# Kernel optimization log

Hardware: AMD Instinct MI355X
Metric: run time of the kernel (lower is better)

The kernel has to match this reference:

```python
import jax, jax.numpy as jnp
import numpy as np

B, NB, H, E, NCT, NL = 16, 4096, 128, 65536, 32, 2
LN_EPS = 1e-5


def _layernorm(x, scale, bias):
    mu = jnp.mean(x, axis=-1, keepdims=True)
    var = jnp.var(x, axis=-1, keepdims=True)
    return (x - mu) / jnp.sqrt(var + LN_EPS) * scale + bias


def setup_inputs() -> dict:
    key = jax.random.key(0)
    ks = jax.random.split(key, 18)
    s = 1.0 / np.sqrt(H)
    inp = {
        'block_tokens': jax.random.normal(ks[0], (B, NB, H), jnp.float32),
        'edge_structure': jnp.full((E,), 0.5, jnp.float32),
        'ct_emb': 0.1 * jax.random.normal(ks[1], (NCT, E), jnp.float32),
        'W_proj': s * jax.random.normal(ks[2], (H, H), jnp.float32),
        'b_proj': jnp.zeros((H,), jnp.float32),
        'W_gate': (1.0 / np.sqrt(2 * H)) * jax.random.normal(ks[3], (2 * H, H), jnp.float32),
        'b_gate': jnp.zeros((H,), jnp.float32),
        'ln_scale': jnp.ones((NL, H), jnp.float32),
        'ln_bias': jnp.zeros((NL, H), jnp.float32),
        'W1': s * jax.random.normal(ks[4], (NL, H, 2 * H), jnp.float32),
        'b1': jnp.zeros((NL, 2 * H), jnp.float32),
        'W2': (1.0 / np.sqrt(2 * H)) * jax.random.normal(ks[5], (NL, 2 * H, H), jnp.float32),
        'b2': jnp.zeros((NL, H), jnp.float32),
        'cancer_type': jax.random.randint(ks[6], (B,), 0, NCT),
        'edge_src': jax.random.randint(ks[7], (E,), 0, NB),
        'edge_dst': jax.random.randint(ks[8], (E,), 0, NB),
        'block_active': jax.random.bernoulli(ks[9], 0.9, (B, NB)),
    }
    return inp


def reference(block_tokens, edge_structure, ct_emb, W_proj, b_proj, W_gate, b_gate,
              ln_scale, ln_bias, W1, b1, W2, b2,
              cancer_type, edge_src, edge_dst, block_active):
    # per-edge signed weights, masked by active src/dst blocks  -> (B, E)
    structure = jax.nn.sigmoid(edge_structure)
    edge_w = structure[None, :] * ct_emb[cancer_type]
    edge_w = edge_w * block_active[:, edge_src].astype(edge_w.dtype) \
                    * block_active[:, edge_dst].astype(edge_w.dtype)
    # route projection + ELU
    h_route = jax.nn.elu(jnp.einsum('bnh,hd->bnd', block_tokens, W_proj) + b_proj)
    # gather sources, weight, scatter-add to destinations
    weighted = edge_w[..., None] * h_route[:, edge_src, :]          # (B, E, H)
    messages = jnp.zeros_like(block_tokens).at[:, edge_dst, :].add(weighted)
    # gated residual
    gate = jax.nn.sigmoid(
        jnp.einsum('bnh,hd->bnd', jnp.concatenate([block_tokens, messages], axis=-1), W_gate) + b_gate)
    x = block_tokens + gate * messages
    # norm + FFN layers (dropout is identity at inference)
    for l in range(NL):
        normed = _layernorm(x, ln_scale[l], ln_bias[l])
        h = jax.nn.elu(jnp.einsum('bnh,hf->bnf', normed, W1[l]) + b1[l])
        x = x + jnp.einsum('bnf,fh->bnh', h, W2[l]) + b2[l]
    return (x, edge_w)
```

## Files before the change

### kernel.cpp

```cpp
#include <hip/hip_runtime.h>
#include <hip/hip_bf16.h>

#define BB     16
#define NBLK   4096
#define HD     128
#define NE     65536
#define MTOT   (BB * NBLK)

typedef __attribute__((ext_vector_type(8))) short bf16x8;
typedef __attribute__((ext_vector_type(4))) float f32x4;

__device__ __forceinline__ float bf2f(unsigned short u) {
    union { unsigned int i; float f; } v; v.i = ((unsigned int)u) << 16; return v.f;
}
__device__ __forceinline__ unsigned short f2bf(float f) {
    union { float f; unsigned int i; } v; v.f = f;
    unsigned int u = v.i;
    unsigned int r = u + 0x7FFFu + ((u >> 16) & 1u);
    return (unsigned short)(r >> 16);
}
__device__ __forceinline__ float ldf(const void* p, size_t i, int f32m) {
    return f32m ? ((const float*)p)[i] : bf2f(((const unsigned short*)p)[i]);
}
__device__ __forceinline__ int get_active(const void* p, int i, int mode) {
    switch (mode) {
        case 1:  return ((const unsigned char*)p)[i] != 0;
        case 2:  return ((const unsigned short*)p)[i] != 0;
        case 3:  return ((const float*)p)[i] != 0.f;
        default: return ((const int*)p)[i] != 0;
    }
}
__device__ __forceinline__ float elu_f(float v) {
    const float e = __expf(v);
    return v > 0.f ? v : e - 1.f;
}
__device__ __forceinline__ float sig_f(float v) {
    return 1.f / (1.f + __expf(-v));
}

__global__ void probe_k(const unsigned int* __restrict__ es,
                        const unsigned int* __restrict__ act,
                        int* __restrict__ flags)
{
    const int lane = threadIdx.x;
    const unsigned int v0 = act[lane], v1 = act[64 + lane];
    auto le1  = [](unsigned int v) { return v <= 1u; };
    auto byt  = [](unsigned int v) {
        return ((v & 0xFFu) <= 1u) && (((v >> 8) & 0xFFu) <= 1u) &&
               (((v >> 16) & 0xFFu) <= 1u) && ((v >> 24) <= 1u); };
    auto f32b = [](unsigned int v) { return v == 0u || v == 0x3F800000u; };
    auto bfb  = [](unsigned int v) {
        unsigned short h0 = (unsigned short)(v & 0xFFFFu), h1 = (unsigned short)(v >> 16);
        return (h0 == 0u || h0 == 0x3F80u) && (h1 == 0u || h1 == 0x3F80u); };
    const unsigned long long m_le1 = __ballot(le1(v0) && le1(v1));
    const unsigned long long m_byt = __ballot(byt(v0) && byt(v1));
    const unsigned long long m_f32 = __ballot(f32b(v0) && f32b(v1));
    const unsigned long long m_bf  = __ballot(bfb(v0) && bfb(v1));
    if (lane == 0) {
        flags[0] = (es[0] != 0x3F003F00u) ? 1 : 0;
        const unsigned long long full = ~0ull;
        flags[1] = (m_le1 == full) ? 0
                 : (m_byt == full) ? 1
                 : (m_f32 == full) ? 3
                 : (m_bf  == full) ? 2 : 0;
    }
}

__global__ __launch_bounds__(256) void cvt_k(const void* __restrict__ bt,
                                             unsigned short* __restrict__ bt16,
                                             const int* __restrict__ flags)
{
    const size_t i = ((size_t)blockIdx.x * 256 + threadIdx.x) * 8;
    if (flags[0]) {
        const float* q = (const float*)bt + i;
        f32x4 lo = *(const f32x4*)q;
        f32x4 hi = *(const f32x4*)(q + 4);
        bf16x8 r;
        #pragma unroll
        for (int j = 0; j < 4; ++j) { r[j] = (short)f2bf(lo[j]); r[4 + j] = (short)f2bf(hi[j]); }
        *(bf16x8*)(bt16 + i) = r;
    } else {
        *(bf16x8*)(bt16 + i) = *(const bf16x8*)((const unsigned short*)bt + i);
    }
}

__global__ __launch_bounds__(256) void transpose_k(
    const void* p0, const void* p1, const void* p2, const void* p3,
    const void* p4, const void* p5, unsigned short* __restrict__ wsT,
    const int* __restrict__ flags)
{
    const void* srcs[6]  = {p0, p1, p2, p3, p4, p5};
    const int eoffs[6]   = {0, 0, 0, 32768, 0, 32768};
    const int Ks[6]      = {128, 256, 128, 128, 256, 256};
    const int nsh[6]     = {7,   7,   8,   8,   7,   7};
    const int offs[6]    = {0, 16384, 49152, 81920, 114688, 147456};
    const int f32m = flags[0];
    const int z = blockIdx.y;
    const int K = Ks[z];
    const int Nn = 1 << nsh[z];
    const int idx = blockIdx.x * 256 + threadIdx.x;
    if (idx >= K * Nn) return;
    const int k = idx >> nsh[z];
    const int n = idx & (Nn - 1);
    wsT[offs[z] + n * K + k] = f2bf(ldf(srcs[z], (size_t)eoffs[z] + idx, f32m));
}

__global__ __launch_bounds__(256) void csr_count_k(const int* __restrict__ edst,
                                                   int* __restrict__ cnt)
{
    const int e = blockIdx.x * 256 + threadIdx.x;
    atomicAdd(&cnt[edst[e]], 1);
}

__global__ __launch_bounds__(1024) void csr_scan_k(const int* __restrict__ cnt,
                                                   int* __restrict__ ofs,
                                                   int* __restrict__ cur)
{
    __shared__ int part[1024];
    const int t = threadIdx.x;
    const int4 c = ((const int4*)cnt)[t];
    part[t] = c.x + c.y + c.z + c.w;
    __syncthreads();
    #pragma unroll
    for (int off = 1; off < 1024; off <<= 1) {
        const int v = (t >= off) ? part[t - off] : 0;
        __syncthreads();
        part[t] += v;
        __syncthreads();
    }
    const int base = t ? part[t - 1] : 0;
    int4 o;
    o.x = base; o.y = o.x + c.x; o.z = o.y + c.y; o.w = o.z + c.z;
    ((int4*)ofs)[t] = o;
    ((int4*)cur)[t] = o;
    if (t == 1023) ofs[4096] = part[1023];
}

__global__ __launch_bounds__(256) void csr_fill_k(const int* __restrict__ edst,
                                                  int* __restrict__ cur,
                                                  int* __restrict__ eidx,
                                                  int* __restrict__ pos_e)
{
    const int e = blockIdx.x * 256 + threadIdx.x;
    const int pos = atomicAdd(&cur[edst[e]], 1);
    eidx[pos] = e;
    pos_e[e] = pos;
}

__global__ __launch_bounds__(256) void edge_k(
    const void* __restrict__ es, const void* __restrict__ ctE,
    const int* __restrict__ ctype, const int* __restrict__ esrc, const int* __restrict__ edst,
    const void* __restrict__ act, const int* __restrict__ pos_e,
    float* __restrict__ out_ew, float2* __restrict__ compact,
    const int* __restrict__ flags)
{
    const int f32m = flags[0], am = flags[1];
    const int idx = blockIdx.x * 256 + threadIdx.x;
    const int b = idx >> 16;
    const int e = idx & 65535;
    const int s = esrc[e];
    const float sv  = sig_f(ldf(es, e, f32m));
    const float emb = ldf(ctE, (size_t)ctype[b] * NE + e, f32m);
    const int a1 = get_active(act, b * NBLK + s, am);
    const int a2 = get_active(act, b * NBLK + edst[e], am);
    const float w = (a1 && a2) ? sv * emb : 0.f;
    out_ew[idx] = w;
    compact[((size_t)b << 16) + pos_e[e]] = make_float2(w, __int_as_float(s));
}

__global__ __launch_bounds__(256) void gather_k(
    const float2* __restrict__ compact, const int* __restrict__ ofs,
    const unsigned short* __restrict__ hr, unsigned short* __restrict__ msg)
{
    const int blk = blockIdx.x;
    const int xcd = blk & 7;
    const int i   = blk >> 3;
    const int b   = xcd * 2 + (i & 1);
    const int d   = ((i >> 1) << 2) | (threadIdx.x >> 6);
    const int lane = threadIdx.x & 63;
    const int sub  = lane >> 4;
    const int l15  = lane & 15;
    const int j1 = ofs[d + 1];
    const size_t bbase = (size_t)b * NBLK * HD;
    const float2* cb = compact + ((size_t)b << 16);
    float acc[8];
    #pragma unroll
    for (int i2 = 0; i2 < 8; ++i2) acc[i2] = 0.f;
    int j = ofs[d] + sub;
    float2 c = (j < j1) ? cb[j] : make_float2(0.f, 0.f);
    while (j < j1) {
        const int jn = j + 4;
        const float2 cn = (jn < j1) ? cb[jn] : make_float2(0.f, 0.f);
        if (c.x != 0.f) {
            const int src = __float_as_int(c.y);
            const bf16x8 v = *(const bf16x8*)(hr + bbase + (size_t)src * HD + l15 * 8);
            #pragma unroll
            for (int i2 = 0; i2 < 8; ++i2)
                acc[i2] += c.x * bf2f((unsigned short)v[i2]);
        }
        c = cn; j = jn;
    }
    #pragma unroll
    for (int i2 = 0; i2 < 8; ++i2) {
        acc[i2] += __shfl_xor(acc[i2], 16);
        acc[i2] += __shfl_xor(acc[i2], 32);
    }
    if (sub == 0) {
        bf16x8 o;
        #pragma unroll
        for (int i2 = 0; i2 < 8; ++i2) o[i2] = (short)f2bf(acc[i2]);
        *(bf16x8*)(msg + bbase + (size_t)d * HD + l15 * 8) = o;
    }
}

template<int K, int N, int EPI>
__global__ __launch_bounds__(256) void gemm_k(
    const unsigned short* __restrict__ A,
    const unsigned short* __restrict__ WT,
    const void* __restrict__ bias, long boff,
    unsigned short* __restrict__ outb,
    const int* __restrict__ flags)
{
    constexpr int KI    = K / 32;
    constexpr int NCW   = N / 4;
    constexpr int NTW   = NCW / 16;
    constexpr int TILES = 4;
    constexpr int NBUF  = (K == 128 ? 4 : 2);
    const int f32m = flags[0];
    const int t    = threadIdx.x;
    const int lane = t & 63;
    const int wave = t >> 6;
    const int q    = lane >> 4;
    const int l15  = lane & 15;
    const int n0   = wave * NCW;

    bf16x8 Bf[KI][NTW];
    #pragma unroll
    for (int ki = 0; ki < KI; ++ki)
        #pragma unroll
        for (int nt = 0; nt < NTW; ++nt)
            Bf[ki][nt] = *(const bf16x8*)(WT + (size_t)(n0 + nt * 16 + l15) * K + ki * 32 + q * 8);

    float biasv[NTW];
    #pragma unroll
    for (int nt = 0; nt < NTW; ++nt)
        biasv[nt] = ldf(bias, boff + n0 + nt * 16 + l15, f32m);

    const int tile0 = blockIdx.x * TILES;
    bf16x8 Af[NBUF][KI];
    auto loadA = [&](int tt) {
        const int arow = (tile0 + tt) * 16 + l15;
        #pragma unroll
        for (int ki = 0; ki < KI; ++ki)
            Af[tt % NBUF][ki] = *(const bf16x8*)(A + (size_t)arow * K + ki * 32 + q * 8);
    };
    #pragma unroll
    for (int p = 0; p < NBUF; ++p) loadA(p);

    #pragma unroll
    for (int tt = 0; tt < TILES; ++tt) {
        const int s = tt % NBUF;
        f32x4 acc[NTW];
        #pragma unroll
        for (int i = 0; i < NTW; ++i) acc[i] = (f32x4){0.f, 0.f, 0.f, 0.f};
        #pragma unroll
        for (int ki = 0; ki < KI; ++ki)
            #pragma unroll
            for (int nt = 0; nt < NTW; ++nt)
                acc[nt] = __builtin_amdgcn_mfma_f32_16x16x32_bf16(Af[s][ki], Bf[ki][nt], acc[nt], 0, 0, 0);

        if (tt + NBUF < TILES) loadA(tt + NBUF);

        const int m0 = (tile0 + tt) * 16;
        #pragma unroll
        for (int nt = 0; nt < NTW; ++nt) {
            #pragma unroll
            for (int r = 0; r < 4; ++r) {
                const int row = m0 + q * 4 + r;
                const int col = n0 + nt * 16 + l15;
                const float v = acc[nt][r] + biasv[nt];
                outb[(size_t)row * N + col] = f2bf(elu_f(v));
            }
        }
    }
}

__global__ __launch_bounds__(256) void mega_k(
    const unsigned short* __restrict__ bt16,
    const unsigned short* __restrict__ msg,
    const void* __restrict__ btf,
    const unsigned short* __restrict__ WT,
    const void* __restrict__ bg,
    const void* __restrict__ b1, const void* __restrict__ b2,
    const void* __restrict__ lns, const void* __restrict__ lnb,
    float* __restrict__ xout,
    const int* __restrict__ flags)
{
    constexpr int R = 32;
    __shared__ __align__(16) float          x_lds[R][132];
    __shared__ __align__(16) unsigned short U[R][264];

    const int f32m = flags[0];
    const int t    = threadIdx.x;
    const int lane = t & 63;
    const int wave = t >> 6;
    const int q    = lane >> 4;
    const int l15  = lane & 15;
    const int row0 = blockIdx.x * R;

    const int ng = wave * 32;
    const unsigned short* WgT = WT + 16384;

    bf16x8 Bg[8][2];
    #pragma unroll
    for (int ki = 0; ki < 8; ++ki)
        #pragma unroll
        for (int nt = 0; nt < 2; ++nt)
            Bg[ki][nt] = *(const bf16x8*)(WgT + (size_t)(ng + nt * 16 + l15) * 256 + ki * 32 + q * 8);
    float biasg[2];
    #pragma unroll
    for (int nt = 0; nt < 2; ++nt) biasg[nt] = ldf(bg, ng + nt * 16 + l15, f32m);

    bf16x8 Ag[2][8];
    #pragma unroll
    for (int tt = 0; tt < 2; ++tt) {
        const int arow = row0 + tt * 16 + l15;
        #pragma unroll
        for (int ki = 0; ki < 8; ++ki) {
            const int k = ki * 32 + q * 8;
            Ag[tt][ki] = (k < HD)
                ? *(const bf16x8*)(bt16 + (size_t)arow * HD + k)
                : *(const bf16x8*)(msg  + (size_t)arow * HD + (k - HD));
        }
    }

    float btv[2][2][4], mgv[2][2][4];
    #pragma unroll
    for (int tt = 0; tt < 2; ++tt)
        #pragma unroll
        for (int nt = 0; nt < 2; ++nt)
            #pragma unroll
            for (int r = 0; r < 4; ++r) {
                const size_t gi = (size_t)(row0 + tt * 16 + q * 4 + r) * HD + ng + nt * 16 + l15;
                btv[tt][nt][r] = ldf(btf, gi, f32m);
                mgv[tt][nt][r] = bf2f(msg[gi]);
            }

    #pragma unroll
    for (int tt = 0; tt < 2; ++tt) {
        f32x4 acc[2];
        #pragma unroll
        for (int nt = 0; nt < 2; ++nt) acc[nt] = (f32x4){0.f, 0.f, 0.f, 0.f};
        #pragma unroll
        for (int ki = 0; ki < 8; ++ki)
            #pragma unroll
            for (int nt = 0; nt < 2; ++nt)
                acc[nt] = __builtin_amdgcn_mfma_f32_16x16x32_bf16(Ag[tt][ki], Bg[ki][nt], acc[nt], 0, 0, 0);
        #pragma unroll
        for (int nt = 0; nt < 2; ++nt)
            #pragma unroll
            for (int r = 0; r < 4; ++r) {
                const float g = sig_f(acc[nt][r] + biasg[nt]);
                x_lds[tt * 16 + q * 4 + r][ng + nt * 16 + l15] =
                    btv[tt][nt][r] + g * mgv[tt][nt][r];
            }
    }
    __syncthreads();

    const int rowln = t >> 3;
    const int seg   = t & 7;
    const int n1 = wave * 64;
    const int n2 = wave * 32;

    #pragma unroll
    for (int l = 0; l < 2; ++l) {
        const unsigned short* W1T = WT + (l ? 81920  : 49152);
        const unsigned short* W2T = WT + (l ? 147456 : 114688);
        const long b1o = l ? 256 : 0, b2o = l ? 128 : 0, lno = l ? 128 : 0;

        bf16x8 B1[4][4];
        #pragma unroll
        for (int ki = 0; ki < 4; ++ki)
            #pragma unroll
            for (int nt = 0; nt < 4; ++nt)
                B1[ki][nt] = *(const bf16x8*)(W1T + (size_t)(n1 + nt * 16 + l15) * 128 + ki * 32 + q * 8);
        float bias1[4];
        #pragma unroll
        for (int nt = 0; nt < 4; ++nt) bias1[nt] = ldf(b1, b1o + n1 + nt * 16 + l15, f32m);

        f32x4 xv[4];
        #pragma unroll
        for (int j = 0; j < 4; ++j) xv[j] = *(const f32x4*)&x_lds[rowln][seg * 16 + j * 4];
        float s = 0.f, ss = 0.f;
        #pragma unroll
        for (int j = 0; j < 4; ++j)
            #pragma unroll
            for (int k = 0; k < 4; ++k) { const float v = xv[j][k]; s += v; ss += v * v; }
        #pragma unroll
        for (int off = 1; off < 8; off <<= 1) { s += __shfl_xor(s, off); ss += __shfl_xor(ss, off); }
        const float mu = s * (1.f / 128.f);
        const float rs = rsqrtf(ss * (1.f / 128.f) - mu * mu + 1e-5f);
        bf16x8 nv[2];
        #pragma unroll
        for (int j = 0; j < 4; ++j)
            #pragma unroll
            for (int k = 0; k < 4; ++k) {
                const int col = seg * 16 + j * 4 + k;
                const float nn = (xv[j][k] - mu) * rs * ldf(lns, lno + col, f32m)
                                 + ldf(lnb, lno + col, f32m);
                nv[j >> 1][(j & 1) * 4 + k] = (short)f2bf(nn);
            }
        *(bf16x8*)&U[rowln][seg * 16]     = nv[0];
        *(bf16x8*)&U[rowln][seg * 16 + 8] = nv[1];
        __syncthreads();

        bf16x8 An[2][4];
        #pragma unroll
        for (int tt = 0; tt < 2; ++tt)
            #pragma unroll
            for (int ki = 0; ki < 4; ++ki)
                An[tt][ki] = *(const bf16x8*)&U[tt * 16 + l15][ki * 32 + q * 8];
        __syncthreads();

        #pragma unroll
        for (int tt = 0; tt < 2; ++tt) {
            f32x4 acc[4];
            #pragma unroll
            for (int nt = 0; nt < 4; ++nt) acc[nt] = (f32x4){0.f, 0.f, 0.f, 0.f};
            #pragma unroll
            for (int ki = 0; ki < 4; ++ki)
                #pragma unroll
                for (int nt = 0; nt < 4; ++nt)
                    acc[nt] = __builtin_amdgcn_mfma_f32_16x16x32_bf16(An[tt][ki], B1[ki][nt], acc[nt], 0, 0, 0);
            #pragma unroll
            for (int nt = 0; nt < 4; ++nt)
                #pragma unroll
                for (int r = 0; r < 4; ++r)
                    U[tt * 16 + q * 4 + r][n1 + nt * 16 + l15] =
                        f2bf(elu_f(acc[nt][r] + bias1[nt]));
        }

        bf16x8 B2[8][2];
        #pragma unroll
        for (int ki = 0; ki < 8; ++ki)
            #pragma unroll
            for (int nt = 0; nt < 2; ++nt)
                B2[ki][nt] = *(const bf16x8*)(W2T + (size_t)(n2 + nt * 16 + l15) * 256 + ki * 32 + q * 8);
        float bias2[2];
        #pragma unroll
        for (int nt = 0; nt < 2; ++nt) bias2[nt] = ldf(b2, b2o + n2 + nt * 16 + l15, f32m);
        __syncthreads();

        #pragma unroll
        for (int tt = 0; tt < 2; ++tt) {
            bf16x8 Ah[8];
            #pragma unroll
            for (int ki = 0; ki < 8; ++ki)
                Ah[ki] = *(const bf16x8*)&U[tt * 16 + l15][ki * 32 + q * 8];
            f32x4 acc[2];
            #pragma unroll
            for (int nt = 0; nt < 2; ++nt) acc[nt] = (f32x4){0.f, 0.f, 0.f, 0.f};
            #pragma unroll
            for (int ki = 0; ki < 8; ++ki)
                #pragma unroll
                for (int nt = 0; nt < 2; ++nt)
                    acc[nt] = __builtin_amdgcn_mfma_f32_16x16x32_bf16(Ah[ki], B2[ki][nt], acc[nt], 0, 0, 0);
            #pragma unroll
            for (int nt = 0; nt < 2; ++nt)
                #pragma unroll
                for (int r = 0; r < 4; ++r)
                    x_lds[tt * 16 + q * 4 + r][n2 + nt * 16 + l15] += acc[nt][r] + bias2[nt];
        }
        __syncthreads();
    }

    float* xo = xout + (size_t)row0 * HD;
    #pragma unroll
    for (int j = 0; j < 4; ++j) {
        const int idx = j * 256 + t;
        const int r2  = idx >> 5;
        const int c4  = (idx & 31) * 4;
        *(f32x4*)(xo + (size_t)idx * 4) = *(const f32x4*)&x_lds[r2][c4];
    }
}

extern "C" void kernel_launch(void* const* d_in, const int* in_sizes, int n_in,
                              void* d_out, int out_size, void* d_ws, size_t ws_size,
                              hipStream_t stream)
{
    (void)in_sizes; (void)n_in; (void)out_size; (void)ws_size;

    const void* bt  = d_in[0];
    const void* es  = d_in[1];
    const void* ctE = d_in[2];
    const void* Wp  = d_in[3];
    const void* bp  = d_in[4];
    const void* Wg  = d_in[5];
    const void* bg  = d_in[6];
    const void* lns = d_in[7];
    const void* lnb = d_in[8];
    const void* W1  = d_in[9];
    const void* b1  = d_in[10];
    const void* W2  = d_in[11];
    const void* b2  = d_in[12];
    const int* ctype = (const int*)d_in[13];
    const int* esrc  = (const int*)d_in[14];
    const int* edst  = (const int*)d_in[15];
    const void* act  = d_in[16];

    float* out_x  = (float*)d_out;
    float* out_ew = out_x + (size_t)MTOT * HD;
    float* x = out_x;

    char* ws = (char*)d_ws;
    int*            flags = (int*)ws;
    unsigned short* msg   = (unsigned short*)(ws + 1024);
    unsigned short* bt16  = (unsigned short*)(ws + 1024 + (16ull << 20));
    unsigned short* hr    = (unsigned short*)(ws + 1024 + (32ull << 20));
    char* base48 = ws + 1024 + (48ull << 20);
    int*            cnt     = (int*)(base48);
    int*            ofs     = (int*)(base48 + (16 << 10));
    int*            cur     = (int*)(base48 + (36 << 10));
    int*            eidx    = (int*)(base48 + (52 << 10));
    int*            pos_e   = (int*)(base48 + (308 << 10));
    unsigned short* WT      = (unsigned short*)(base48 + (576 << 10));
    float2*         compact = (float2*)(base48 + (1 << 20));

    const int M = MTOT;

    probe_k<<<1, 64, 0, stream>>>((const unsigned int*)es, (const unsigned int*)act, flags);
    hipMemsetAsync(cnt, 0, NBLK * sizeof(int), stream);

    cvt_k<<<dim3((M * HD / 8) / 256), 256, 0, stream>>>(bt, bt16, flags);
    transpose_k<<<dim3(128, 6), 256, 0, stream>>>(Wp, Wg, W1, W1, W2, W2, WT, flags);

    csr_count_k<<<dim3(NE / 256), 256, 0, stream>>>(edst, cnt);
    csr_scan_k<<<dim3(1), 1024, 0, stream>>>(cnt, ofs, cur);
    csr_fill_k<<<dim3(NE / 256), 256, 0, stream>>>(edst, cur, eidx, pos_e);

    edge_k<<<dim3((BB * NE) / 256), 256, 0, stream>>>(
        es, ctE, ctype, esrc, edst, act, pos_e, out_ew, compact, flags);

    gemm_k<128, 128, 0><<<dim3(M / 64), 256, 0, stream>>>(
        bt16, WT + 0, bp, 0, hr, flags);

    gather_k<<<dim3(M / 4), 256, 0, stream>>>(compact, ofs, hr, msg);

    mega_k<<<dim3(M / 32), 256, 0, stream>>>(
        bt16, msg, bt, WT, bg, b1, b2, lns, lnb, x, flags);
}
```

Before: 321.9 us.

## Process two row tiles per block in fused kernel with swizzled LDS

The fused gate+FFN kernel now handles 64 rows per block as two 32-row sub-tiles, so the per-layer weight fragments, biases and layernorm params loaded into registers are reused across both tiles. Padding in the LDS arrays is replaced by an XOR-like rotation swizzle to avoid bank conflicts, and MFMA loops are wrapped with s_setprio. The projection GEMM also doubles rows per block. This halves weight reloads and grid size but raises LDS use and may reduce occupancy and parallelism.

```diff
diff --git a/kernel.cpp b/kernel.cpp
--- a/kernel.cpp
+++ b/kernel.cpp
@@ -224,7 +224,7 @@
     constexpr int KI    = K / 32;
     constexpr int NCW   = N / 4;
     constexpr int NTW   = NCW / 16;
-    constexpr int TILES = 4;
+    constexpr int TILES = 8;
     constexpr int NBUF  = (K == 128 ? 4 : 2);
     const int f32m = flags[0];
     const int t    = threadIdx.x;
@@ -284,6 +284,9 @@
         }
     }
 }
+
+#define XI(tl, row, col)  x_lds[tl][row][((col) + 4 * (row)) & 127]
+#define UIx(row, col)     U[row][((col) + 8 * (row)) & 255]
 
 __global__ __launch_bounds__(256) void mega_k(
     const unsigned short* __restrict__ bt16,
@@ -296,9 +299,8 @@
     float* __restrict__ xout,
     const int* __restrict__ flags)
 {
-    constexpr int R = 32;
-    __shared__ __align__(16) float          x_lds[R][132];
-    __shared__ __align__(16) unsigned short U[R][264];
+    __shared__ __align__(16) float          x_lds[2][32][128];
+    __shared__ __align__(16) unsigned short U[32][256];
 
     const int f32m = flags[0];
     const int t    = threadIdx.x;
@@ -306,7 +308,7 @@
     const int wave = t >> 6;
     const int q    = lane >> 4;
     const int l15  = lane & 15;
-    const int row0 = blockIdx.x * R;
+    const int base = blockIdx.x * 64;
 
     const int ng = wave * 32;
     const unsigned short* WgT = WT + 16384;
@@ -321,49 +323,53 @@
     #pragma unroll
     for (int nt = 0; nt < 2; ++nt) biasg[nt] = ldf(bg, ng + nt * 16 + l15, f32m);
 
-    bf16x8 Ag[2][8];
-    #pragma unroll
-    for (int tt = 0; tt < 2; ++tt) {
-        const int arow = row0 + tt * 16 + l15;
-        #pragma unroll
-        for (int ki = 0; ki < 8; ++ki) {
-            const int k = ki * 32 + q * 8;
-            Ag[tt][ki] = (k < HD)
-                ? *(const bf16x8*)(bt16 + (size_t)arow * HD + k)
-                : *(const bf16x8*)(msg  + (size_t)arow * HD + (k - HD));
+    #pragma unroll
+    for (int tl = 0; tl < 2; ++tl) {
+        const int row0 = base + tl * 32;
+        bf16x8 Ag[2][8];
+        #pragma unroll
+        for (int tt = 0; tt < 2; ++tt) {
+            const int arow = row0 + tt * 16 + l15;
+            #pragma unroll
+            for (int ki = 0; ki < 8; ++ki) {
+                const int k = ki * 32 + q * 8;
+                Ag[tt][ki] = (k < HD)
+                    ? *(const bf16x8*)(bt16 + (size_t)arow * HD + k)
+                    : *(const bf16x8*)(msg  + (size_t)arow * HD + (k - HD));
+            }
         }
-    }
-
-    float btv[2][2][4], mgv[2][2][4];
-    #pragma unroll
-    for (int tt = 0; tt < 2; ++tt)
-        #pragma unroll
-        for (int nt = 0; nt < 2; ++nt)
-            #pragma unroll
-            for (int r = 0; r < 4; ++r) {
-                const size_t gi = (size_t)(row0 + tt * 16 + q * 4 + r) * HD + ng + nt * 16 + l15;
-                btv[tt][nt][r] = ldf(btf, gi, f32m);
-                mgv[tt][nt][r] = bf2f(msg[gi]);
-            }
-
-    #pragma unroll
-    for (int tt = 0; tt < 2; ++tt) {
-        f32x4 acc[2];
-        #pragma unroll
-        for (int nt = 0; nt < 2; ++nt) acc[nt] = (f32x4){0.f, 0.f, 0.f, 0.f};
-        #pragma unroll
-        for (int ki = 0; ki < 8; ++ki)
+        float btv[2][2][4], mgv[2][2][4];
+        #pragma unroll
+        for (int tt = 0; tt < 2; ++tt)
             #pragma unroll
             for (int nt = 0; nt < 2; ++nt)
-                acc[nt] = __builtin_amdgcn_mfma_f32_16x16x32_bf16(Ag[tt][ki], Bg[ki][nt], acc[nt], 0, 0, 0);
-        #pragma unroll
-        for (int nt = 0; nt < 2; ++nt)
-            #pragma unroll
-            for (int r = 0; r < 4; ++r) {
-                const float g = sig_f(acc[nt][r] + biasg[nt]);
-                x_lds[tt * 16 + q * 4 + r][ng + nt * 16 + l15] =
-                    btv[tt][nt][r] + g * mgv[tt][nt][r];
-            }
+                #pragma unroll
+                for (int r = 0; r < 4; ++r) {
+                    const size_t gi = (size_t)(row0 + tt * 16 + q * 4 + r) * HD + ng + nt * 16 + l15;
+                    btv[tt][nt][r] = ldf(btf, gi, f32m);
+                    mgv[tt][nt][r] = bf2f(msg[gi]);
+                }
+        #pragma unroll
+        for (int tt = 0; tt < 2; ++tt) {
+            f32x4 acc[2];
+            #pragma unroll
+            for (int nt = 0; nt < 2; ++nt) acc[nt] = (f32x4){0.f, 0.f, 0.f, 0.f};
+            __builtin_amdgcn_s_setprio(1);
+            #pragma unroll
+            for (int ki = 0; ki < 8; ++ki)
+                #pragma unroll
+                for (int nt = 0; nt < 2; ++nt)
+                    acc[nt] = __builtin_amdgcn_mfma_f32_16x16x32_bf16(Ag[tt][ki], Bg[ki][nt], acc[nt], 0, 0, 0);
+            __builtin_amdgcn_s_setprio(0);
+            #pragma unroll
+            for (int nt = 0; nt < 2; ++nt)
+                #pragma unroll
+                for (int r = 0; r < 4; ++r) {
+                    const float g = sig_f(acc[nt][r] + biasg[nt]);
+                    XI(tl, tt * 16 + q * 4 + r, ng + nt * 16 + l15) =
+                        btv[tt][nt][r] + g * mgv[tt][nt][r];
+                }
+        }
     }
     __syncthreads();
 
@@ -387,59 +393,6 @@
         float bias1[4];
         #pragma unroll
         for (int nt = 0; nt < 4; ++nt) bias1[nt] = ldf(b1, b1o + n1 + nt * 16 + l15, f32m);
-
-        f32x4 xv[4];
-        #pragma unroll
-        for (int j = 0; j < 4; ++j) xv[j] = *(const f32x4*)&x_lds[rowln][seg * 16 + j * 4];
-        float s = 0.f, ss = 0.f;
-        #pragma unroll
-        for (int j = 0; j < 4; ++j)
-            #pragma unroll
-            for (int k = 0; k < 4; ++k) { const float v = xv[j][k]; s += v; ss += v * v; }
-        #pragma unroll
-        for (int off = 1; off < 8; off <<= 1) { s += __shfl_xor(s, off); ss += __shfl_xor(ss, off); }
-        const float mu = s * (1.f / 128.f);
-        const float rs = rsqrtf(ss * (1.f / 128.f) - mu * mu + 1e-5f);
-        bf16x8 nv[2];
-        #pragma unroll
-        for (int j = 0; j < 4; ++j)
-            #pragma unroll
-            for (int k = 0; k < 4; ++k) {
-                const int col = seg * 16 + j * 4 + k;
-                const float nn = (xv[j][k] - mu) * rs * ldf(lns, lno + col, f32m)
-                                 + ldf(lnb, lno + col, f32m);
-                nv[j >> 1][(j & 1) * 4 + k] = (short)f2bf(nn);
-            }
-        *(bf16x8*)&U[rowln][seg * 16]     = nv[0];
-        *(bf16x8*)&U[rowln][seg * 16 + 8] = nv[1];
-        __syncthreads();
-
-        bf16x8 An[2][4];
-        #pragma unroll
-        for (int tt = 0; tt < 2; ++tt)
-            #pragma unroll
-            for (int ki = 0; ki < 4; ++ki)
-                An[tt][ki] = *(const bf16x8*)&U[tt * 16 + l15][ki * 32 + q * 8];
-        __syncthreads();
-
-        #pragma unroll
-        for (int tt = 0; tt < 2; ++tt) {
-            f32x4 acc[4];
-            #pragma unroll
-            for (int nt = 0; nt < 4; ++nt) acc[nt] = (f32x4){0.f, 0.f, 0.f, 0.f};
-            #pragma unroll
-            for (int ki = 0; ki < 4; ++ki)
-                #pragma unroll
-                for (int nt = 0; nt < 4; ++nt)
-                    acc[nt] = __builtin_amdgcn_mfma_f32_16x16x32_bf16(An[tt][ki], B1[ki][nt], acc[nt], 0, 0, 0);
-            #pragma unroll
-            for (int nt = 0; nt < 4; ++nt)
-                #pragma unroll
-                for (int r = 0; r < 4; ++r)
-                    U[tt * 16 + q * 4 + r][n1 + nt * 16 + l15] =
-                        f2bf(elu_f(acc[nt][r] + bias1[nt]));
-        }
-
         bf16x8 B2[8][2];
         #pragma unroll
         for (int ki = 0; ki < 8; ++ki)
@@ -449,38 +402,109 @@
         float bias2[2];
         #pragma unroll
         for (int nt = 0; nt < 2; ++nt) bias2[nt] = ldf(b2, b2o + n2 + nt * 16 + l15, f32m);
-        __syncthreads();
-
-        #pragma unroll
-        for (int tt = 0; tt < 2; ++tt) {
-            bf16x8 Ah[8];
-            #pragma unroll
-            for (int ki = 0; ki < 8; ++ki)
-                Ah[ki] = *(const bf16x8*)&U[tt * 16 + l15][ki * 32 + q * 8];
-            f32x4 acc[2];
-            #pragma unroll
-            for (int nt = 0; nt < 2; ++nt) acc[nt] = (f32x4){0.f, 0.f, 0.f, 0.f};
-            #pragma unroll
-            for (int ki = 0; ki < 8; ++ki)
+
+        float lsv[16], lbv[16];
+        #pragma unroll
+        for (int j = 0; j < 4; ++j)
+            #pragma unroll
+            for (int k = 0; k < 4; ++k) {
+                const int col = seg * 16 + j * 4 + k;
+                lsv[j * 4 + k] = ldf(lns, lno + col, f32m);
+                lbv[j * 4 + k] = ldf(lnb, lno + col, f32m);
+            }
+
+        #pragma unroll
+        for (int tl = 0; tl < 2; ++tl) {
+            f32x4 xv[4];
+            #pragma unroll
+            for (int j = 0; j < 4; ++j)
+                xv[j] = *(const f32x4*)&XI(tl, rowln, seg * 16 + j * 4);
+            float s = 0.f, ss = 0.f;
+            #pragma unroll
+            for (int j = 0; j < 4; ++j)
+                #pragma unroll
+                for (int k = 0; k < 4; ++k) { const float v = xv[j][k]; s += v; ss += v * v; }
+            #pragma unroll
+            for (int off = 1; off < 8; off <<= 1) { s += __shfl_xor(s, off); ss += __shfl_xor(ss, off); }
+            const float mu = s * (1.f / 128.f);
+            const float rs = rsqrtf(ss * (1.f / 128.f) - mu * mu + 1e-5f);
+            bf16x8 nv[2];
+            #pragma unroll
+            for (int j = 0; j < 4; ++j)
+                #pragma unroll
+                for (int k = 0; k < 4; ++k) {
+                    const float nn = (xv[j][k] - mu) * rs * lsv[j * 4 + k] + lbv[j * 4 + k];
+                    nv[j >> 1][(j & 1) * 4 + k] = (short)f2bf(nn);
+                }
+            *(bf16x8*)&UIx(rowln, seg * 16)     = nv[0];
+            *(bf16x8*)&UIx(rowln, seg * 16 + 8) = nv[1];
+            __syncthreads();
+
+            bf16x8 An[2][4];
+            #pragma unroll
+            for (int tt = 0; tt < 2; ++tt)
+                #pragma unroll
+                for (int ki = 0; ki < 4; ++ki)
+                    An[tt][ki] = *(const bf16x8*)&UIx(tt * 16 + l15, ki * 32 + q * 8);
+            __syncthreads();
+
+            #pragma unroll
+            for (int tt = 0; tt < 2; ++tt) {
+                f32x4 acc[4];
+                #pragma unroll
+                for (int nt = 0; nt < 4; ++nt) acc[nt] = (f32x4){0.f, 0.f, 0.f, 0.f};
+                __builtin_amdgcn_s_setprio(1);
+                #pragma unroll
+                for (int ki = 0; ki < 4; ++ki)
+                    #pragma unroll
+                    for (int nt = 0; nt < 4; ++nt)
+                        acc[nt] = __builtin_amdgcn_mfma_f32_16x16x32_bf16(An[tt][ki], B1[ki][nt], acc[nt], 0, 0, 0);
+                __builtin_amdgcn_s_setprio(0);
+                #pragma unroll
+                for (int nt = 0; nt < 4; ++nt)
+                    #pragma unroll
+                    for (int r = 0; r < 4; ++r)
+                        UIx(tt * 16 + q * 4 + r, n1 + nt * 16 + l15) =
+                            f2bf(elu_f(acc[nt][r] + bias1[nt]));
+            }
+            __syncthreads();
+
+            #pragma unroll
+            for (int tt = 0; tt < 2; ++tt) {
+                bf16x8 Ah[8];
+                #pragma unroll
+                for (int ki = 0; ki < 8; ++ki)
+                    Ah[ki] = *(const bf16x8*)&UIx(tt * 16 + l15, ki * 32 + q * 8);
+                f32x4 acc[2];
+                #pragma unroll
+                for (int nt = 0; nt < 2; ++nt) acc[nt] = (f32x4){0.f, 0.f, 0.f, 0.f};
+                __builtin_amdgcn_s_setprio(1);
+                #pragma unroll
+                for (int ki = 0; ki < 8; ++ki)
+                    #pragma unroll
+                    for (int nt = 0; nt < 2; ++nt)
+                        acc[nt] = __builtin_amdgcn_mfma_f32_16x16x32_bf16(Ah[ki], B2[ki][nt], acc[nt], 0, 0, 0);
+                __builtin_amdgcn_s_setprio(0);
                 #pragma unroll
                 for (int nt = 0; nt < 2; ++nt)
-                    acc[nt] = __builtin_amdgcn_mfma_f32_16x16x32_bf16(Ah[ki], B2[ki][nt], acc[nt], 0, 0, 0);
-            #pragma unroll
-            for (int nt = 0; nt < 2; ++nt)
-                #pragma unroll
-                for (int r = 0; r < 4; ++r)
-                    x_lds[tt * 16 + q * 4 + r][n2 + nt * 16 + l15] += acc[nt][r] + bias2[nt];
+                    #pragma unroll
+                    for (int r = 0; r < 4; ++r)
+                        XI(tl, tt * 16 + q * 4 + r, n2 + nt * 16 + l15) += acc[nt][r] + bias2[nt];
+            }
+            __syncthreads();
         }
-        __syncthreads();
-    }
-
-    float* xo = xout + (size_t)row0 * HD;
-    #pragma unroll
-    for (int j = 0; j < 4; ++j) {
-        const int idx = j * 256 + t;
-        const int r2  = idx >> 5;
-        const int c4  = (idx & 31) * 4;
-        *(f32x4*)(xo + (size_t)idx * 4) = *(const f32x4*)&x_lds[r2][c4];
+    }
+
+    #pragma unroll
+    for (int tl = 0; tl < 2; ++tl) {
+        float* xo = xout + (size_t)(base + tl * 32) * HD;
+        #pragma unroll
+        for (int j = 0; j < 4; ++j) {
+            const int idx = j * 256 + t;
+            const int r2  = idx >> 5;
+            const int c4  = (idx & 31) * 4;
+            *(f32x4*)(xo + (size_t)idx * 4) = *(const f32x4*)&XI(tl, r2, c4);
+        }
     }
 }
 
@@ -541,11 +565,11 @@
     edge_k<<<dim3((BB * NE) / 256), 256, 0, stream>>>(
         es, ctE, ctype, esrc, edst, act, pos_e, out_ew, compact, flags);
 
-    gemm_k<128, 128, 0><<<dim3(M / 64), 256, 0, stream>>>(
+    gemm_k<128, 128, 0><<<dim3(M / 128), 256, 0, stream>>>(
         bt16, WT + 0, bp, 0, hr, flags);
 
     gather_k<<<dim3(M / 4), 256, 0, stream>>>(compact, ofs, hr, msg);
 
-    mega_k<<<dim3(M / 32), 256, 0, stream>>>(
+    mega_k<<<dim3(M / 64), 256, 0, stream>>>(
         bt16, msg, bt, WT, bg, b1, b2, lns, lnb, x, flags);
 }
```

Measured after the change: 315.8 us. Within noise of the previous version (-1.9%).
